# Kernel optimization log

Hardware: AMD Instinct MI355X
Metric: run time of the kernel (lower is better)

The kernel has to match this reference:

```python
import jax, jax.numpy as jnp
import numpy as np
from jax import lax

T_MAX, BATCH, CLASSES, L_MAX = 512, 32, 1296, 64
NINF = -jnp.inf


def _align_one(logsm, label, C, R):
    """Monotonic max-probability forced alignment for one sample.
    logsm: [T, V] log-probs, label: [L] int, C=x_len (valid frames), R=label_len.
    Returns per-frame pseudo target [T] (0-padded past C)."""
    T, V = logsm.shape
    L = label.shape[0]
    rows = jnp.arange(L)
    cols = jnp.arange(T)
    # pb[i, j] = logsm[j, label[i]], restricted to the monotonic band i <= j <= C-R+i
    pb = logsm[:, label].T  # [L, T]
    band = (cols[None, :] >= rows[:, None]) & (cols[None, :] <= C - R + rows[:, None]) & (rows[:, None] < R)
    pb = jnp.where(band, pb, NINF)

    # Forward DP over time columns: dp[i,j] = max(dp[i-1,j-1], dp[i,j-1]) + pb[i,j]
    # (strict > for the diagonal move, exactly as the original numpy code).
    dp0 = jnp.where(rows == 0, pb[:, 0], NINF)

    def step(dp, pb_col):
        shifted = jnp.concatenate([jnp.full((1,), NINF, dp.dtype), dp[:-1]])
        choice = shifted > dp  # True -> came from (i-1, j-1)
        dp_new = jnp.where(choice, shifted, dp) + pb_col
        return dp_new, choice

    _, choices = lax.scan(step, dp0, pb.T[1:])  # [T-1, L] bool
    choices = jnp.concatenate([jnp.zeros((1, L), bool), choices], axis=0)  # [T, L]

    # Backtrack from (R-1, C-1); columns j >= C emit padding 0.
    def bstep(row, jc):
        j, ch = jc
        active = j < C
        tgt = jnp.where(active, label[row], 0)
        row_new = jnp.where(active, row - ch[row].astype(row.dtype), row)
        return row_new, tgt

    row0 = (R - 1).astype(jnp.int32)
    _, targets = lax.scan(bstep, row0, (jnp.arange(T), choices), reverse=True)
    return targets  # [T]


def _make_targets(logsm, label, x_len, label_len):
    # logsm: [T, B, V] -> targets [T, B]
    return jax.vmap(_align_one, in_axes=(1, 0, 0, 0))(logsm, label, x_len, label_len).T


def setup_inputs() -> dict:
    key = jax.random.key(0)
    k0, k1, k2, k3, k4 = jax.random.split(key, 5)
    pred = jax.random.normal(k0, (T_MAX, BATCH, CLASSES), jnp.float32)
    seq_pred = jax.random.normal(k1, (T_MAX, BATCH, CLASSES), jnp.float32)
    label = jax.random.randint(k2, (BATCH, L_MAX), 0, CLASSES)
    x_len = jax.random.randint(k3, (BATCH,), T_MAX // 2, T_MAX + 1)  # >= L_MAX so band is valid
    label_len = jax.random.randint(k4, (BATCH,), 8, L_MAX + 1)
    return {"pred": pred, "seq_pred": seq_pred, "label": label, "x_len": x_len, "label_len": label_len}


def reference(pred, seq_pred, label, x_len, label_len):
    T, B, V = pred.shape
    logsm_seq = jax.nn.log_softmax(seq_pred, axis=-1)
    target = _make_targets(logsm_seq, label, x_len, label_len)  # [T, B] int
    probs = jnp.exp(logsm_seq)  # softmax(seq_pred)
    conf = jnp.take_along_axis(probs, target[..., None], axis=2)[..., 0]  # [T, B]
    smooth = (1.0 - conf) / (V - 1)
    onehot = jax.nn.one_hot(target, V, dtype=pred.dtype)  # [T, B, V]
    true_dist = jnp.where(onehot > 0, conf[..., None], smooth[..., None])
    mask = (jnp.arange(T)[:, None] < x_len[None, :]).astype(pred.dtype)  # [T, B]
    ce = jnp.sum(-true_dist * jax.nn.log_softmax(pred, axis=-1), axis=-1) * mask
    return jnp.mean(ce)
```

## Files before the change

### kernel.cpp

```cpp
#include <hip/hip_runtime.h>

#define T_MAX 512
#define BATCH 32
#define CLASSES 1296
#define L_MAX 64
#define NROWS (T_MAX * BATCH)
#define NINF (-INFINITY)
#define NSEQBLK (NROWS / 8)
#define NPREDBLK (NROWS / 8)

__device__ __forceinline__ float wave_sum64(float v) {
    v += __int_as_float(__builtin_amdgcn_update_dpp(0, __float_as_int(v), 0x111, 0xF, 0xF, true));
    v += __int_as_float(__builtin_amdgcn_update_dpp(0, __float_as_int(v), 0x112, 0xF, 0xF, true));
    v += __int_as_float(__builtin_amdgcn_update_dpp(0, __float_as_int(v), 0x114, 0xF, 0xF, true));
    v += __int_as_float(__builtin_amdgcn_update_dpp(0, __float_as_int(v), 0x118, 0xF, 0xF, true));
    v += __int_as_float(__builtin_amdgcn_update_dpp(0, __float_as_int(v), 0x142, 0xF, 0xF, true));
    v += __int_as_float(__builtin_amdgcn_update_dpp(0, __float_as_int(v), 0x143, 0xF, 0xF, true));
    return v;
}

__global__ __launch_bounds__(512, 4) void stream_kernel(
    const float* __restrict__ pred, const float* __restrict__ seqp,
    const int* __restrict__ label,
    float* __restrict__ lse_pred, float* __restrict__ sum_pred,
    float* __restrict__ lse_seq, float* __restrict__ pb,
    int* __restrict__ counter)
{
    __shared__ float rowbuf[8][CLASSES];
    const int w = threadIdx.x >> 6, lane = threadIdx.x & 63;
    if (blockIdx.x == 0 && threadIdx.x == 0) *counter = 0;

    if (blockIdx.x < NSEQBLK) {
        const int r = (blockIdx.x << 3) + w;
        const int b = r & 31, t = r >> 5;
        const float* xs = seqp + (size_t)r * CLASSES;
        const float4* s4 = (const float4*)xs;

        float4 b0 = s4[lane],       b1 = s4[lane + 64],  b2 = s4[lane + 128];
        float4 b3 = s4[lane + 192], b4 = s4[lane + 256];
        float4 bt = make_float4(0.f, 0.f, 0.f, 0.f);
        if (lane < 4) bt = s4[320 + lane];
        const int lab = label[(b << 6) + lane];

        float4* rb4 = (float4*)rowbuf[w];
        rb4[lane] = b0; rb4[lane + 64] = b1; rb4[lane + 128] = b2;
        rb4[lane + 192] = b3; rb4[lane + 256] = b4;
        if (lane < 4) rb4[320 + lane] = bt;

        float ss = __expf(b0.x) + __expf(b0.y) + __expf(b0.z) + __expf(b0.w)
                 + __expf(b1.x) + __expf(b1.y) + __expf(b1.z) + __expf(b1.w)
                 + __expf(b2.x) + __expf(b2.y) + __expf(b2.z) + __expf(b2.w)
                 + __expf(b3.x) + __expf(b3.y) + __expf(b3.z) + __expf(b3.w)
                 + __expf(b4.x) + __expf(b4.y) + __expf(b4.z) + __expf(b4.w);
        if (lane < 4)
            ss += __expf(bt.x) + __expf(bt.y) + __expf(bt.z) + __expf(bt.w);
        ss = wave_sum64(ss);
        if (lane == 63) lse_seq[r] = __logf(ss);

        pb[(((size_t)(b << 9) + t) << 6) + lane] = rowbuf[w][lab];
    } else {
        const int r = ((blockIdx.x - NSEQBLK) << 3) + w;
        const float* xp = pred + (size_t)r * CLASSES;
        const float4* p4 = (const float4*)xp;

        float4 a0 = p4[lane],       a1 = p4[lane + 64],  a2 = p4[lane + 128];
        float4 a3 = p4[lane + 192], a4 = p4[lane + 256];
        float4 at = make_float4(0.f, 0.f, 0.f, 0.f);
        if (lane < 4) at = p4[320 + lane];

        float sp = __expf(a0.x) + __expf(a0.y) + __expf(a0.z) + __expf(a0.w)
                 + __expf(a1.x) + __expf(a1.y) + __expf(a1.z) + __expf(a1.w)
                 + __expf(a2.x) + __expf(a2.y) + __expf(a2.z) + __expf(a2.w)
                 + __expf(a3.x) + __expf(a3.y) + __expf(a3.z) + __expf(a3.w)
                 + __expf(a4.x) + __expf(a4.y) + __expf(a4.z) + __expf(a4.w);
        float sx = (a0.x + a0.y + a0.z + a0.w) + (a1.x + a1.y + a1.z + a1.w)
                 + (a2.x + a2.y + a2.z + a2.w) + (a3.x + a3.y + a3.z + a3.w)
                 + (a4.x + a4.y + a4.z + a4.w);
        if (lane < 4) {
            sp += __expf(at.x) + __expf(at.y) + __expf(at.z) + __expf(at.w);
            sx += at.x + at.y + at.z + at.w;
        }
        sp = wave_sum64(sp);
        sx = wave_sum64(sx);
        if (lane == 63) {
            lse_pred[r] = __logf(sp);
            sum_pred[r] = sx;
        }
    }
}

__global__ __launch_bounds__(512, 2) void align_ce_kernel(
    const float* __restrict__ pred, const float* __restrict__ pb,
    const int* __restrict__ label, const int* __restrict__ x_len,
    const int* __restrict__ label_len,
    const float* __restrict__ lse_pred, const float* __restrict__ sum_pred,
    const float* __restrict__ lse_seq,
    float* __restrict__ partials, int* __restrict__ counter,
    float* __restrict__ out)
{
    __shared__ unsigned chw[8][1024];
    __shared__ int a_s[8][64];
    __shared__ int rows_s[8][T_MAX];
    __shared__ float sm[8];
    const int w = threadIdx.x >> 6, lane = threadIdx.x & 63;

    const int b = (blockIdx.x << 3) + w;
    const int C = x_len[b], R = label_len[b];
    const int limit = C - R;
    const float* pbb = pb + ((size_t)b << 15);
    const int P = (C + 31) >> 5;
    const int G = P << 1;
    const float biasR = (lane < R) ? 0.f : NINF;
    const bool isb0 = (lane & 15) == 0;
    const int ninf_i = 0xFF800000;
    unsigned* chwl = chw[w];

    float bA[16], bB[16], bC[16], bD[16];
    float dp = NINF;
    unsigned w0 = 0;

#define GLOAD(VV, GG) {                                                        \
        int gi_ = (GG); if (gi_ > G - 1) gi_ = G - 1;                          \
        const float* s_ = pbb + ((size_t)gi_ << 10);                           \
        _Pragma("unroll")                                                      \
        for (int u = 0; u < 16; ++u) VV[u] = s_[(u << 6) + lane];              \
    }

#define COMPUTE16(VV, GG) {                                                    \
        const int g_ = (GG);                                                   \
        const bool general = (g_ < 2) || (((g_ << 4) + 15) > limit);           \
        _Pragma("unroll")                                                      \
        for (int u = 0; u < 16; ++u) {                                         \
            const int j = (g_ << 4) + u;                                       \
            float val;                                                         \
            if (general) {                                                     \
                if (g_ == 0 && u == 0) {                    \
                    dp = (lane == 0) ? VV[0] : NINF;                           \
                    continue;                                                  \
                }                                                              \
                const bool ib = (lane <= j) && (lane >= j - limit) && (lane < R); \
                val = ib ? VV[u] : NINF;                                       \
            } else {                                                           \
                val = VV[u] + biasR;                     \
            }                                                                  \
            const int dpb = __float_as_int(dp);                                \
            const int t1 = __builtin_amdgcn_update_dpp(ninf_i, dpb, 0x111, 0xF, 0xF, false);  \
            const int t2 = __builtin_amdgcn_update_dpp(ninf_i, dpb, 0x142, 0xF, 0xF, false);  \
            const float shifted = __int_as_float(isb0 ? t2 : t1);              \
            const bool c = shifted > dp;                \
            w0 |= (c ? 1u : 0u) << (j & 31);                                   \
            dp = fmaxf(shifted, dp) + val;            \
        }                                                                      \
    }

    GLOAD(bA, 0) GLOAD(bB, 1) GLOAD(bC, 2)
    for (int g = 0; g < G; g += 4) {
        GLOAD(bD, g + 3)
        COMPUTE16(bA, g)
        GLOAD(bA, g + 4)
        COMPUTE16(bB, g + 1)
        chwl[((g >> 1) << 6) + lane] = w0; w0 = 0;
        if (g + 2 < G) {
            GLOAD(bB, g + 5)
            COMPUTE16(bC, g + 2)
            GLOAD(bC, g + 6)
            COMPUTE16(bD, g + 3)
            chwl[(((g >> 1) + 1) << 6) + lane] = w0; w0 = 0;
        }
    }
#undef GLOAD
#undef COMPUTE16

    if (lane == 0) {
        int row = R - 1, j = C - 1;
        while (row > 0 && j >= 0) {
            unsigned word = chwl[((j >> 5) << 6) + row];
            unsigned mb = (2u << (j & 31)) - 1;
            unsigned m = word & mb;
            if (m) {
                int hb = 31 - __clz(m);
                int aj = (j & ~31) | hb;
                a_s[w][row] = aj;
                row--; j = aj - 1;
            } else {
                j = (j & ~31) - 1;
            }
        }
        for (int i = row; i >= 0; --i) a_s[w][i] = 0;
    }
    if (lane < R) {
        int a = a_s[w][lane];
        int bi = (lane == R - 1) ? (C - 1) : (a_s[w][lane + 1] - 1);
        for (int j = a; j <= bi; ++j) rows_s[w][j] = lane;
    }

    float ces = 0.f;
    #pragma unroll
    for (int k = 0; k < 8; ++k) {
        const int t = (k << 6) + lane;
        if (t < C) {
            const int e = (t << 5) + b;
            const int row = rows_s[w][t];
            const int tgt = label[(b << 6) + row];
            const float lp = lse_pred[e];
            const float S = sum_pred[e] - (float)CLASSES * lp;
            const float lsp_t = pred[(size_t)e * CLASSES + tgt] - lp;
            const float conf = __expf(pb[(((size_t)(b << 9) + t) << 6) + row] - lse_seq[e]);
            const float smooth = (1.f - conf) * (1.f / (float)(CLASSES - 1));
            ces += -((conf - smooth) * lsp_t + smooth * S);
        }
    }
    ces = wave_sum64(ces);
    if (lane == 63) sm[w] = ces;
    __syncthreads();
    if (threadIdx.x == 0) {
        float p = sm[0] + sm[1] + sm[2] + sm[3] + sm[4] + sm[5] + sm[6] + sm[7];
        __hip_atomic_store(&partials[blockIdx.x], p, __ATOMIC_RELEASE, __HIP_MEMORY_SCOPE_AGENT);
        if (__hip_atomic_fetch_add(counter, 1, __ATOMIC_ACQ_REL, __HIP_MEMORY_SCOPE_AGENT) == 3) {
            float v = 0.f;
            for (int i = 0; i < 4; ++i)
                v += __hip_atomic_load(&partials[i], __ATOMIC_ACQUIRE, __HIP_MEMORY_SCOPE_AGENT);
            out[0] = v * (1.0f / (float)NROWS);
        }
    }
}

extern "C" void kernel_launch(void* const* d_in, const int* in_sizes, int n_in,
                              void* d_out, int out_size, void* d_ws, size_t ws_size,
                              hipStream_t stream) {
    const float* pred      = (const float*)d_in[0];
    const float* seq_pred  = (const float*)d_in[1];
    const int*   label     = (const int*)d_in[2];
    const int*   x_len     = (const int*)d_in[3];
    const int*   label_len = (const int*)d_in[4];
    float* out = (float*)d_out;

    float* ws = (float*)d_ws;
    float* lse_pred = ws;
    float* sum_pred = ws + NROWS;
    float* lse_seq  = ws + 2 * NROWS;
    float* pb       = ws + 3 * NROWS;
    float* partials = pb + (size_t)BATCH * T_MAX * 64;
    int*   counter  = (int*)(partials + 4);

    stream_kernel<<<NSEQBLK + NPREDBLK, 512, 0, stream>>>(
        pred, seq_pred, label, lse_pred, sum_pred, lse_seq, pb, counter);
    align_ce_kernel<<<4, 512, 0, stream>>>(
        pred, pb, label, x_len, label_len,
        lse_pred, sum_pred, lse_seq, partials, counter, out);
}
```

Before: 232.5 us.

## Overlap alignment DP with pred streaming in a fused kernel

Splits the streaming kernel so only the seq_pred pass runs first. The second kernel pairs 32 per-sample alignment blocks with the pred log-sum-exp blocks, so the serial DP runs while pred is being streamed. The DP blocks stage band data into LDS with global_load_lds through a three-deep ring and spin on a completion counter before the CE step. This adds a spin-wait dependency between blocks of the same launch, which could deadlock if the alignment blocks occupied every slot, and it trades the per-block many-wave layout for one DP wave per block.

```diff
diff --git a/kernel.cpp b/kernel.cpp
--- a/kernel.cpp
+++ b/kernel.cpp
@@ -6,8 +6,8 @@
 #define L_MAX 64
 #define NROWS (T_MAX * BATCH)
 #define NINF (-INFINITY)
-#define NSEQBLK (NROWS / 8)
-#define NPREDBLK (NROWS / 8)
+#define NSEQBLK 2048
+#define NPREDBLK 2048
 
 __device__ __forceinline__ float wave_sum64(float v) {
     v += __int_as_float(__builtin_amdgcn_update_dpp(0, __float_as_int(v), 0x111, 0xF, 0xF, true));
@@ -19,47 +19,62 @@
     return v;
 }
 
-__global__ __launch_bounds__(512, 4) void stream_kernel(
-    const float* __restrict__ pred, const float* __restrict__ seqp,
-    const int* __restrict__ label,
-    float* __restrict__ lse_pred, float* __restrict__ sum_pred,
+__global__ __launch_bounds__(512, 4) void seq_kernel(
+    const float* __restrict__ seqp, const int* __restrict__ label,
     float* __restrict__ lse_seq, float* __restrict__ pb,
-    int* __restrict__ counter)
+    int* __restrict__ predDone, int* __restrict__ partCnt)
 {
     __shared__ float rowbuf[8][CLASSES];
     const int w = threadIdx.x >> 6, lane = threadIdx.x & 63;
-    if (blockIdx.x == 0 && threadIdx.x == 0) *counter = 0;
-
-    if (blockIdx.x < NSEQBLK) {
-        const int r = (blockIdx.x << 3) + w;
-        const int b = r & 31, t = r >> 5;
-        const float* xs = seqp + (size_t)r * CLASSES;
-        const float4* s4 = (const float4*)xs;
-
-        float4 b0 = s4[lane],       b1 = s4[lane + 64],  b2 = s4[lane + 128];
-        float4 b3 = s4[lane + 192], b4 = s4[lane + 256];
-        float4 bt = make_float4(0.f, 0.f, 0.f, 0.f);
-        if (lane < 4) bt = s4[320 + lane];
-        const int lab = label[(b << 6) + lane];
-
-        float4* rb4 = (float4*)rowbuf[w];
-        rb4[lane] = b0; rb4[lane + 64] = b1; rb4[lane + 128] = b2;
-        rb4[lane + 192] = b3; rb4[lane + 256] = b4;
-        if (lane < 4) rb4[320 + lane] = bt;
-
-        float ss = __expf(b0.x) + __expf(b0.y) + __expf(b0.z) + __expf(b0.w)
-                 + __expf(b1.x) + __expf(b1.y) + __expf(b1.z) + __expf(b1.w)
-                 + __expf(b2.x) + __expf(b2.y) + __expf(b2.z) + __expf(b2.w)
-                 + __expf(b3.x) + __expf(b3.y) + __expf(b3.z) + __expf(b3.w)
-                 + __expf(b4.x) + __expf(b4.y) + __expf(b4.z) + __expf(b4.w);
-        if (lane < 4)
-            ss += __expf(bt.x) + __expf(bt.y) + __expf(bt.z) + __expf(bt.w);
-        ss = wave_sum64(ss);
-        if (lane == 63) lse_seq[r] = __logf(ss);
-
-        pb[(((size_t)(b << 9) + t) << 6) + lane] = rowbuf[w][lab];
-    } else {
-        const int r = ((blockIdx.x - NSEQBLK) << 3) + w;
+    if (blockIdx.x == 0 && threadIdx.x == 0) { *predDone = 0; *partCnt = 0; }
+
+    const int r = (blockIdx.x << 3) + w;
+    const int b = r & 31, t = r >> 5;
+    const float* xs = seqp + (size_t)r * CLASSES;
+    const float4* s4 = (const float4*)xs;
+
+    float4 b0 = s4[lane],       b1 = s4[lane + 64],  b2 = s4[lane + 128];
+    float4 b3 = s4[lane + 192], b4 = s4[lane + 256];
+    float4 bt = make_float4(0.f, 0.f, 0.f, 0.f);
+    if (lane < 4) bt = s4[320 + lane];
+    const int lab = label[(b << 6) + lane];
+
+    float4* rb4 = (float4*)rowbuf[w];
+    rb4[lane] = b0; rb4[lane + 64] = b1; rb4[lane + 128] = b2;
+    rb4[lane + 192] = b3; rb4[lane + 256] = b4;
+    if (lane < 4) rb4[320 + lane] = bt;
+
+    float ss = __expf(b0.x) + __expf(b0.y) + __expf(b0.z) + __expf(b0.w)
+             + __expf(b1.x) + __expf(b1.y) + __expf(b1.z) + __expf(b1.w)
+             + __expf(b2.x) + __expf(b2.y) + __expf(b2.z) + __expf(b2.w)
+             + __expf(b3.x) + __expf(b3.y) + __expf(b3.z) + __expf(b3.w)
+             + __expf(b4.x) + __expf(b4.y) + __expf(b4.z) + __expf(b4.w);
+    if (lane < 4)
+        ss += __expf(bt.x) + __expf(bt.y) + __expf(bt.z) + __expf(bt.w);
+    ss = wave_sum64(ss);
+    if (lane == 63) lse_seq[r] = __logf(ss);
+
+    pb[(((size_t)(b << 9) + t) << 6) + lane] = rowbuf[w][lab];
+}
+
+__global__ __launch_bounds__(512, 2) void fused_kernel(
+    const float* __restrict__ pred, const float* __restrict__ pb,
+    const int* __restrict__ label, const int* __restrict__ x_len,
+    const int* __restrict__ label_len,
+    float* __restrict__ lse_pred, float* __restrict__ sum_pred,
+    const float* __restrict__ lse_seq,
+    float* __restrict__ partials, int* __restrict__ predDone,
+    int* __restrict__ partCnt, float* __restrict__ out)
+{
+    __shared__ float ring[3][64 * 64];
+    __shared__ unsigned chw[16][64];
+    __shared__ int a_s[64];
+    __shared__ int rows_s[T_MAX];
+    __shared__ float sm[8];
+    const int w = threadIdx.x >> 6, lane = threadIdx.x & 63;
+
+    if (blockIdx.x >= 32) {
+        const int r = ((blockIdx.x - 32) << 3) + w;
         const float* xp = pred + (size_t)r * CLASSES;
         const float4* p4 = (const float4*)xp;
 
@@ -83,142 +98,139 @@
         sp = wave_sum64(sp);
         sx = wave_sum64(sx);
         if (lane == 63) {
-            lse_pred[r] = __logf(sp);
-            sum_pred[r] = sx;
-        }
-    }
-}
-
-__global__ __launch_bounds__(512, 2) void align_ce_kernel(
-    const float* __restrict__ pred, const float* __restrict__ pb,
-    const int* __restrict__ label, const int* __restrict__ x_len,
-    const int* __restrict__ label_len,
-    const float* __restrict__ lse_pred, const float* __restrict__ sum_pred,
-    const float* __restrict__ lse_seq,
-    float* __restrict__ partials, int* __restrict__ counter,
-    float* __restrict__ out)
-{
-    __shared__ unsigned chw[8][1024];
-    __shared__ int a_s[8][64];
-    __shared__ int rows_s[8][T_MAX];
-    __shared__ float sm[8];
-    const int w = threadIdx.x >> 6, lane = threadIdx.x & 63;
-
-    const int b = (blockIdx.x << 3) + w;
+            __hip_atomic_store(&lse_pred[r], __logf(sp), __ATOMIC_RELAXED, __HIP_MEMORY_SCOPE_AGENT);
+            __hip_atomic_store(&sum_pred[r], sx, __ATOMIC_RELAXED, __HIP_MEMORY_SCOPE_AGENT);
+        }
+        __syncthreads();
+        if (threadIdx.x == 0)
+            __hip_atomic_fetch_add(predDone, 1, __ATOMIC_RELEASE, __HIP_MEMORY_SCOPE_AGENT);
+        return;
+    }
+
+    const int b = blockIdx.x;
     const int C = x_len[b], R = label_len[b];
     const int limit = C - R;
     const float* pbb = pb + ((size_t)b << 15);
     const int P = (C + 31) >> 5;
-    const int G = P << 1;
+    const int SS = (P + 1) >> 1;
     const float biasR = (lane < R) ? 0.f : NINF;
     const bool isb0 = (lane & 15) == 0;
     const int ninf_i = 0xFF800000;
-    unsigned* chwl = chw[w];
-
-    float bA[16], bB[16], bC[16], bD[16];
-    float dp = NINF;
-    unsigned w0 = 0;
-
-#define GLOAD(VV, GG) {                                                        \
-        int gi_ = (GG); if (gi_ > G - 1) gi_ = G - 1;                          \
-        const float* s_ = pbb + ((size_t)gi_ << 10);                           \
+
+    if (w == 0) {
+        float dp = NINF;
+
+#define STAGE(S) { const int s_ = (S); if (s_ < SS) {                          \
+        const char* src_ = (const char*)pbb + ((size_t)s_ << 14) + lane * 16;  \
+        float* dst_ = ring[s_ % 3];                                            \
         _Pragma("unroll")                                                      \
-        for (int u = 0; u < 16; ++u) VV[u] = s_[(u << 6) + lane];              \
-    }
-
-#define COMPUTE16(VV, GG) {                                                    \
-        const int g_ = (GG);                                                   \
-        const bool general = (g_ < 2) || (((g_ << 4) + 15) > limit);           \
-        _Pragma("unroll")                                                      \
-        for (int u = 0; u < 16; ++u) {                                         \
-            const int j = (g_ << 4) + u;                                       \
-            float val;                                                         \
-            if (general) {                                                     \
-                if (g_ == 0 && u == 0) {                    \
-                    dp = (lane == 0) ? VV[0] : NINF;                           \
-                    continue;                                                  \
-                }                                                              \
-                const bool ib = (lane <= j) && (lane >= j - limit) && (lane < R); \
-                val = ib ? VV[u] : NINF;                                       \
-            } else {                                                           \
-                val = VV[u] + biasR;                     \
-            }                                                                  \
-            const int dpb = __float_as_int(dp);                                \
-            const int t1 = __builtin_amdgcn_update_dpp(ninf_i, dpb, 0x111, 0xF, 0xF, false);  \
-            const int t2 = __builtin_amdgcn_update_dpp(ninf_i, dpb, 0x142, 0xF, 0xF, false);  \
-            const float shifted = __int_as_float(isb0 ? t2 : t1);              \
-            const bool c = shifted > dp;                \
-            w0 |= (c ? 1u : 0u) << (j & 31);                                   \
-            dp = fmaxf(shifted, dp) + val;            \
-        }                                                                      \
-    }
-
-    GLOAD(bA, 0) GLOAD(bB, 1) GLOAD(bC, 2)
-    for (int g = 0; g < G; g += 4) {
-        GLOAD(bD, g + 3)
-        COMPUTE16(bA, g)
-        GLOAD(bA, g + 4)
-        COMPUTE16(bB, g + 1)
-        chwl[((g >> 1) << 6) + lane] = w0; w0 = 0;
-        if (g + 2 < G) {
-            GLOAD(bB, g + 5)
-            COMPUTE16(bC, g + 2)
-            GLOAD(bC, g + 6)
-            COMPUTE16(bD, g + 3)
-            chwl[(((g >> 1) + 1) << 6) + lane] = w0; w0 = 0;
-        }
-    }
-#undef GLOAD
-#undef COMPUTE16
-
-    if (lane == 0) {
-        int row = R - 1, j = C - 1;
-        while (row > 0 && j >= 0) {
-            unsigned word = chwl[((j >> 5) << 6) + row];
-            unsigned mb = (2u << (j & 31)) - 1;
-            unsigned m = word & mb;
-            if (m) {
-                int hb = 31 - __clz(m);
-                int aj = (j & ~31) | hb;
-                a_s[w][row] = aj;
-                row--; j = aj - 1;
-            } else {
-                j = (j & ~31) - 1;
+        for (int k = 0; k < 16; ++k)                                           \
+            __builtin_amdgcn_global_load_lds(                                  \
+                (const __attribute__((address_space(1))) void*)(src_ + (k << 10)), \
+                (__attribute__((address_space(3))) void*)(dst_ + (k << 8)), 16, 0, 0); } }
+
+        STAGE(0) STAGE(1) STAGE(2)
+        for (int s = 0; s < SS; ++s) {
+            asm volatile("s_waitcnt vmcnt(32)" ::: "memory");
+            const float* sp_ = ring[s % 3];
+            #pragma unroll
+            for (int half = 0; half < 2; ++half) {
+                const int pp = (s << 1) + half;
+                if (pp >= P) break;
+                unsigned w0 = 0;
+                #pragma unroll
+                for (int g = 0; g < 2; ++g) {
+                    const int g_ = (pp << 1) + g;
+                    float v[16];
+                    #pragma unroll
+                    for (int u = 0; u < 16; ++u)
+                        v[u] = sp_[(((half << 1) + g) << 4) * 64 + (u << 6) + lane];
+                    const bool general = (g_ < 2) || (((g_ << 4) + 15) > limit);
+                    #pragma unroll
+                    for (int u = 0; u < 16; ++u) {
+                        const int kk = (g << 4) + u;
+                        const int j = (g_ << 4) + u;
+                        float val;
+                        if (general) {
+                            if (g_ == 0 && u == 0) {
+                                dp = (lane == 0) ? v[0] : NINF;
+                                continue;
+                            }
+                            const bool ib = (lane <= j) && (lane >= j - limit) && (lane < R);
+                            val = ib ? v[u] : NINF;
+                        } else {
+                            val = v[u] + biasR;
+                        }
+                        const int dpb = __float_as_int(dp);
+                        const int t1 = __builtin_amdgcn_update_dpp(ninf_i, dpb, 0x111, 0xF, 0xF, false);
+                        const int t2 = __builtin_amdgcn_update_dpp(ninf_i, dpb, 0x142, 0xF, 0xF, false);
+                        const float shifted = __int_as_float(isb0 ? t2 : t1);
+                        const bool c = shifted > dp;
+                        w0 |= (c ? 1u : 0u) << kk;
+                        dp = fmaxf(shifted, dp) + val;
+                    }
+                }
+                chw[pp][lane] = w0;
             }
-        }
-        for (int i = row; i >= 0; --i) a_s[w][i] = 0;
-    }
-    if (lane < R) {
-        int a = a_s[w][lane];
-        int bi = (lane == R - 1) ? (C - 1) : (a_s[w][lane + 1] - 1);
-        for (int j = a; j <= bi; ++j) rows_s[w][j] = lane;
-    }
-
-    float ces = 0.f;
-    #pragma unroll
-    for (int k = 0; k < 8; ++k) {
-        const int t = (k << 6) + lane;
-        if (t < C) {
-            const int e = (t << 5) + b;
-            const int row = rows_s[w][t];
-            const int tgt = label[(b << 6) + row];
-            const float lp = lse_pred[e];
-            const float S = sum_pred[e] - (float)CLASSES * lp;
-            const float lsp_t = pred[(size_t)e * CLASSES + tgt] - lp;
-            const float conf = __expf(pb[(((size_t)(b << 9) + t) << 6) + row] - lse_seq[e]);
-            const float smooth = (1.f - conf) * (1.f / (float)(CLASSES - 1));
-            ces += -((conf - smooth) * lsp_t + smooth * S);
-        }
-    }
-    ces = wave_sum64(ces);
-    if (lane == 63) sm[w] = ces;
+            STAGE(s + 3)
+        }
+        asm volatile("s_waitcnt vmcnt(0)" ::: "memory");
+#undef STAGE
+
+        if (lane == 0) {
+            int row = R - 1, j = C - 1;
+            while (row > 0 && j >= 0) {
+                unsigned word = chw[j >> 5][row];
+                unsigned mb = (2u << (j & 31)) - 1;
+                unsigned m = word & mb;
+                if (m) {
+                    int hb = 31 - __clz(m);
+                    int aj = (j & ~31) | hb;
+                    a_s[row] = aj;
+                    row--; j = aj - 1;
+                } else {
+                    j = (j & ~31) - 1;
+                }
+            }
+            for (int i = row; i >= 0; --i) a_s[i] = 0;
+        }
+        if (lane < R) {
+            int a = a_s[lane];
+            int bi = (lane == R - 1) ? (C - 1) : (a_s[lane + 1] - 1);
+            for (int j = a; j <= bi; ++j) rows_s[j] = lane;
+        }
+    }
+    __syncthreads();
+
+    if (threadIdx.x == 0) {
+        while (__hip_atomic_load(predDone, __ATOMIC_ACQUIRE, __HIP_MEMORY_SCOPE_AGENT) < NPREDBLK)
+            __builtin_amdgcn_s_sleep(8);
+    }
+    __syncthreads();
+
+    const int t = threadIdx.x;
+    float ce = 0.f;
+    if (t < C) {
+        const int e = (t << 5) + b;
+        const int row = rows_s[t];
+        const int tgt = label[(b << 6) + row];
+        const float lp = __hip_atomic_load(&lse_pred[e], __ATOMIC_RELAXED, __HIP_MEMORY_SCOPE_AGENT);
+        const float sx = __hip_atomic_load(&sum_pred[e], __ATOMIC_RELAXED, __HIP_MEMORY_SCOPE_AGENT);
+        const float S = sx - (float)CLASSES * lp;
+        const float lsp_t = pred[(size_t)e * CLASSES + tgt] - lp;
+        const float conf = __expf(pbb[((size_t)t << 6) + row] - lse_seq[e]);
+        const float smooth = (1.f - conf) * (1.f / (float)(CLASSES - 1));
+        ce = -((conf - smooth) * lsp_t + smooth * S);
+    }
+    ce = wave_sum64(ce);
+    if (lane == 63) sm[w] = ce;
     __syncthreads();
     if (threadIdx.x == 0) {
         float p = sm[0] + sm[1] + sm[2] + sm[3] + sm[4] + sm[5] + sm[6] + sm[7];
-        __hip_atomic_store(&partials[blockIdx.x], p, __ATOMIC_RELEASE, __HIP_MEMORY_SCOPE_AGENT);
-        if (__hip_atomic_fetch_add(counter, 1, __ATOMIC_ACQ_REL, __HIP_MEMORY_SCOPE_AGENT) == 3) {
+        __hip_atomic_store(&partials[b], p, __ATOMIC_RELEASE, __HIP_MEMORY_SCOPE_AGENT);
+        if (__hip_atomic_fetch_add(partCnt, 1, __ATOMIC_ACQ_REL, __HIP_MEMORY_SCOPE_AGENT) == 31) {
             float v = 0.f;
-            for (int i = 0; i < 4; ++i)
+            for (int i = 0; i < 32; ++i)
                 v += __hip_atomic_load(&partials[i], __ATOMIC_ACQUIRE, __HIP_MEMORY_SCOPE_AGENT);
             out[0] = v * (1.0f / (float)NROWS);
         }
@@ -241,11 +253,12 @@
     float* lse_seq  = ws + 2 * NROWS;
     float* pb       = ws + 3 * NROWS;
     float* partials = pb + (size_t)BATCH * T_MAX * 64;
-    int*   counter  = (int*)(partials + 4);
-
-    stream_kernel<<<NSEQBLK + NPREDBLK, 512, 0, stream>>>(
-        pred, seq_pred, label, lse_pred, sum_pred, lse_seq, pb, counter);
-    align_ce_kernel<<<4, 512, 0, stream>>>(
+    int*   predDone = (int*)(partials + 32);
+    int*   partCnt  = predDone + 1;
+
+    seq_kernel<<<NSEQBLK, 512, 0, stream>>>(seq_pred, label, lse_seq, pb,
+                                            predDone, partCnt);
+    fused_kernel<<<32 + NPREDBLK, 512, 0, stream>>>(
         pred, pb, label, x_len, label_len,
-        lse_pred, sum_pred, lse_seq, partials, counter, out);
-}
+        lse_pred, sum_pred, lse_seq, partials, predDone, partCnt, out);
+}
```

After: 281.5 us. 1.21x slower.
